# Kernel tuning notes

Hardware: AMD Instinct MI355X
Metric: run time of the kernel (lower is better)

The kernel has to match this reference:

```python
import jax, jax.numpy as jnp
from jax import lax
import numpy as np

NH, KA = 8, 3            # num_heads, local kernel size
C_HID = 64               # adapter hidden dim (== SlideAttention dim)
C_RED = C_HID // 4       # dim_reduction=4 -> 16
C_H = C_RED // NH        # channels per head after reduction -> 2
SCALE = float((C_HID // NH) ** -0.5)  # head_dim=8 scaling


def _shift_kernel(dtype):
    # fixed 'shift' depthwise kernel: output tap i picks neighbor (i//3, i%3)
    base = np.zeros((KA * KA, 1, KA, KA), np.float32)
    for i in range(KA * KA):
        base[i, 0, i // KA, i % KA] = 1.0
    return jnp.asarray(np.tile(base, (C_H, 1, 1, 1)), dtype)


def _dwconv(x, w, b):
    # depthwise grouped conv: (G, C_H, H, W) -> (G, C_H*9, H, W)
    y = lax.conv_general_dilated(x, w, (1, 1), 'SAME',
                                 dimension_numbers=('NCHW', 'OIHW', 'NCHW'),
                                 feature_group_count=C_H)
    return y + b[None, :, None, None]


def _forward(x, fc1_w, fc1_b, conv_w, conv_b, qkv_w, qkv_b, dep1_w, dep_b,
             dep1_b, rpb, proj_w, proj_b, fc2_w, fc2_b):
    B, L, _ = x.shape
    pw = lambda h, w, b: jnp.einsum('blc,oc->blo', h, w) + b  # 1x1 conv1d == pointwise linear
    xs = pw(x, fc1_w, fc1_b)                                   # (B,L,64)
    h = pw(pw(xs, conv_w[0], conv_b[0]), conv_w[1], conv_b[1])  # A,B (dropout=eval identity)
    h = pw(pw(h, conv_w[2], conv_b[2]), conv_w[3], conv_b[3])   # C,D
    h = pw(pw(h, conv_w[4], conv_b[4]), conv_w[5], conv_b[5])   # E,F
    h = pw(pw(h, conv_w[6], conv_b[6]), conv_w[7], conv_b[7]) + h  # G,H + residual (scale=1)
    xs = jax.nn.gelu(h, approximate=False)                     # nn.GELU default (erf)
    Hh, Ww, C = B, L, C_HID
    x4 = xs.reshape(1, C, Hh, Ww)                              # raw torch.reshape semantics
    # ---- SlideAttention (dim=64, heads=8, ka=3, dim_reduction=4, rpb) ----
    xp = jnp.transpose(x4, (0, 2, 3, 1))                       # (1,H,W,C)
    qkv = xp @ qkv_w.T + qkv_b                                 # (1,H,W,3*C_RED)
    f = jnp.transpose(qkv, (0, 3, 1, 2)).reshape(NH, 3 * C_H, Hh, Ww)
    q, k, v = f[:, :C_H], f[:, C_H:2 * C_H], f[:, 2 * C_H:]
    sw = _shift_kernel(x.dtype)
    k = _dwconv(k, sw, dep_b) + _dwconv(k, dep1_w, dep1_b)     # shared dwc kernels
    v = _dwconv(v, sw, dep_b) + _dwconv(v, dep1_w, dep1_b)
    q6 = q.reshape(1, NH, C_H, 1, Hh, Ww)
    k6 = k.reshape(1, NH, C_H, KA * KA, Hh, Ww) + rpb          # relative position bias
    v6 = v.reshape(1, NH, C_H, KA * KA, Hh, Ww)
    attn = jax.nn.softmax(jnp.sum(q6 * SCALE * k6, axis=2, keepdims=True), axis=3)
    o = jnp.sum(attn * v6, axis=3).reshape(1, C_RED, Hh, Ww)   # (1,16,H,W)
    o = jnp.transpose(o, (0, 2, 3, 1)) @ proj_w.T + proj_b     # (1,H,W,64)
    o = jnp.transpose(o, (0, 3, 1, 2))                         # (1,C,H,W)
    xs = o.reshape(Hh, Ww, C)                                  # raw reshape back
    out = xs @ fc2_w.T + fc2_b                                 # D_fc2: 64 -> 768
    return x + out                                             # skip connection


def setup_inputs() -> dict:
    ks = jax.random.split(jax.random.key(0), 16)
    f32 = jnp.float32
    n = lambda k, s, sc: jax.random.normal(k, s, f32) * sc
    return {
        'x': jax.random.normal(ks[0], (32, 2048, 768), f32),
        'fc1_w': n(ks[1], (64, 768), 0.05), 'fc1_b': n(ks[2], (64,), 0.02),
        'conv_w': n(ks[3], (8, 64, 64), 0.1), 'conv_b': n(ks[4], (8, 64), 0.02),
        'qkv_w': n(ks[5], (48, 64), 0.1), 'qkv_b': n(ks[6], (48,), 0.02),
        'dep1_w': n(ks[7], (18, 1, 3, 3), 0.1),
        'dep_b': n(ks[8], (18,), 0.02), 'dep1_b': n(ks[9], (18,), 0.02),
        'rpb': n(ks[10], (1, 8, 1, 9, 1, 1), 0.02),
        'proj_w': n(ks[11], (64, 16), 0.1), 'proj_b': n(ks[12], (64,), 0.02),
        'fc2_w': n(ks[13], (768, 64), 0.05), 'fc2_b': n(ks[14], (768,), 0.02),
    }


def reference(x, fc1_w, fc1_b, conv_w, conv_b, qkv_w, qkv_b, dep1_w, dep_b,
              dep1_b, rpb, proj_w, proj_b, fc2_w, fc2_b):
    return _forward(x, fc1_w, fc1_b, conv_w, conv_b, qkv_w, qkv_b, dep1_w,
                    dep_b, dep1_b, rpb, proj_w, proj_b, fc2_w, fc2_b)
```

## Files before the change

kernel.cpp:

```cpp
#include <hip/hip_runtime.h>
#include <math.h>

__device__ __forceinline__ int SW64(int ch, int t)  { return (ch << 6) + (t ^ (ch & 28)); }
__device__ __forceinline__ int SW128(int ch, int t) { return (ch << 7) + (t ^ (ch & 28)); }

__global__ __launch_bounds__(256, 4) void k_fc1_chain(
    const float* __restrict__ x, const float* __restrict__ fc1_w,
    const float* __restrict__ fc1_b, const float* __restrict__ conv_w,
    const float* __restrict__ conv_b, float* __restrict__ xs)
{
    __shared__ float lds[2 * 4096];
    float* bufA = lds;
    float* bufB = lds + 4096;

    const int tid = threadIdx.x;
    const int tx = tid & 15;
    const int ty = tid >> 4;
    const int t0 = blockIdx.x * 64;
    const int c0 = tx * 4;
    const int r0 = ty * 4;

    float acc[4][4];
#pragma unroll
    for (int i = 0; i < 4; ++i)
#pragma unroll
        for (int j = 0; j < 4; ++j) acc[i][j] = 0.f;

    float xr[4][4], wr1[4][4];
#pragma unroll
    for (int i = 0; i < 4; ++i) {
        const float4 v = *(const float4*)(x + (size_t)(t0 + r0 + i) * 768 + c0);
        xr[i][0] = v.x; xr[i][1] = v.y; xr[i][2] = v.z; xr[i][3] = v.w;
        const float4 u = *(const float4*)(fc1_w + (size_t)(r0 + i) * 768 + c0);
        wr1[i][0] = u.x; wr1[i][1] = u.y; wr1[i][2] = u.z; wr1[i][3] = u.w;
    }

    for (int k0 = 0; k0 < 768; k0 += 64) {
#pragma unroll
        for (int j = 0; j < 4; ++j) {
            float4 s; s.x = xr[0][j]; s.y = xr[1][j]; s.z = xr[2][j]; s.w = xr[3][j];
            *(float4*)(bufA + SW64(c0 + j, r0)) = s;
            float4 t; t.x = wr1[0][j]; t.y = wr1[1][j]; t.z = wr1[2][j]; t.w = wr1[3][j];
            *(float4*)(bufB + SW64(c0 + j, r0)) = t;
        }
        __syncthreads();

        if (k0 + 64 < 768) {
#pragma unroll
            for (int i = 0; i < 4; ++i) {
                const float4 v = *(const float4*)(x + (size_t)(t0 + r0 + i) * 768 + k0 + 64 + c0);
                xr[i][0] = v.x; xr[i][1] = v.y; xr[i][2] = v.z; xr[i][3] = v.w;
                const float4 u = *(const float4*)(fc1_w + (size_t)(r0 + i) * 768 + k0 + 64 + c0);
                wr1[i][0] = u.x; wr1[i][1] = u.y; wr1[i][2] = u.z; wr1[i][3] = u.w;
            }
        }

#pragma unroll 16
        for (int k = 0; k < 64; ++k) {
            const float4 a4 = *(const float4*)(bufA + SW64(k, r0));
            const float4 b4 = *(const float4*)(bufB + SW64(k, c0));
            const float a[4] = {a4.x, a4.y, a4.z, a4.w};
            const float b[4] = {b4.x, b4.y, b4.z, b4.w};
#pragma unroll
            for (int i = 0; i < 4; ++i)
#pragma unroll
                for (int j = 0; j < 4; ++j) acc[i][j] = fmaf(a[i], b[j], acc[i][j]);
        }
        __syncthreads();
    }

#pragma unroll
    for (int j = 0; j < 4; ++j) {
        const float b = fc1_b[c0 + j];
        float4 s;
        s.x = acc[0][j] + b; s.y = acc[1][j] + b;
        s.z = acc[2][j] + b; s.w = acc[3][j] + b;
        *(float4*)(bufA + SW64(c0 + j, r0)) = s;
    }
    {
        float wr[4][4];
#pragma unroll
        for (int i = 0; i < 4; ++i) {
            const float4 v = *(const float4*)(conv_w + (r0 + i) * 64 + c0);
            wr[i][0] = v.x; wr[i][1] = v.y; wr[i][2] = v.z; wr[i][3] = v.w;
        }
#pragma unroll
        for (int j = 0; j < 4; ++j) {
            float4 s; s.x = wr[0][j]; s.y = wr[1][j]; s.z = wr[2][j]; s.w = wr[3][j];
            *(float4*)(bufB + SW64(c0 + j, r0)) = s;
        }
    }
    __syncthreads();

    float* cur = bufA;
    float* wb  = bufB;
    float res[4][4];

    for (int l = 0; l < 8; ++l) {
        float wr[4][4];
        if (l < 7) {
#pragma unroll
            for (int i = 0; i < 4; ++i) {
                const float4 v = *(const float4*)(conv_w + (l + 1) * 4096 + (r0 + i) * 64 + c0);
                wr[i][0] = v.x; wr[i][1] = v.y; wr[i][2] = v.z; wr[i][3] = v.w;
            }
        }
#pragma unroll
        for (int i = 0; i < 4; ++i)
#pragma unroll
            for (int j = 0; j < 4; ++j) acc[i][j] = 0.f;
#pragma unroll 16
        for (int k = 0; k < 64; ++k) {
            const float4 a4 = *(const float4*)(cur + SW64(k, r0));
            const float4 b4 = *(const float4*)(wb + SW64(k, c0));
            const float a[4] = {a4.x, a4.y, a4.z, a4.w};
            const float b[4] = {b4.x, b4.y, b4.z, b4.w};
#pragma unroll
            for (int i = 0; i < 4; ++i)
#pragma unroll
                for (int j = 0; j < 4; ++j) acc[i][j] = fmaf(a[i], b[j], acc[i][j]);
        }
#pragma unroll
        for (int i = 0; i < 4; ++i)
#pragma unroll
            for (int j = 0; j < 4; ++j) acc[i][j] += conv_b[l * 64 + c0 + j];

        if (l == 5) {
#pragma unroll
            for (int i = 0; i < 4; ++i)
#pragma unroll
                for (int j = 0; j < 4; ++j) res[i][j] = acc[i][j];
        }
        if (l < 7) {
            __syncthreads();
#pragma unroll
            for (int j = 0; j < 4; ++j) {
                float4 s; s.x = acc[0][j]; s.y = acc[1][j]; s.z = acc[2][j]; s.w = acc[3][j];
                *(float4*)(wb + SW64(c0 + j, r0)) = s;
                float4 t; t.x = wr[0][j]; t.y = wr[1][j]; t.z = wr[2][j]; t.w = wr[3][j];
                *(float4*)(cur + SW64(c0 + j, r0)) = t;
            }
            float* tmp = cur; cur = wb; wb = tmp;
            __syncthreads();
        }
    }

#pragma unroll
    for (int i = 0; i < 4; ++i) {
        float4 g4;
        float v;
        v = acc[i][0] + res[i][0]; g4.x = 0.5f * v * (1.f + erff(v * 0.70710678118654752f));
        v = acc[i][1] + res[i][1]; g4.y = 0.5f * v * (1.f + erff(v * 0.70710678118654752f));
        v = acc[i][2] + res[i][2]; g4.z = 0.5f * v * (1.f + erff(v * 0.70710678118654752f));
        v = acc[i][3] + res[i][3]; g4.w = 0.5f * v * (1.f + erff(v * 0.70710678118654752f));
        *(float4*)(xs + (size_t)(t0 + r0 + i) * 64 + c0) = g4;
    }
}

__global__ __launch_bounds__(256) void k_qkv(
    const float* __restrict__ xs, const float* __restrict__ qkv_w,
    const float* __restrict__ qkv_b, float* __restrict__ qkv)
{
    __shared__ float wq[12 * 64];
    __shared__ float qb[12];
    const int tid = threadIdx.x;
    const int g = blockIdx.y;
    for (int i = tid; i < 768; i += 256) wq[i] = qkv_w[g * 768 + i];
    if (tid < 12) qb[tid] = qkv_b[g * 12 + tid];
    __syncthreads();

    const int p = blockIdx.x * 256 + tid;
    float acc[12];
#pragma unroll
    for (int n = 0; n < 12; ++n) acc[n] = qb[n];

    for (int c = 0; c < 64; c += 4) {
        const float xv0 = xs[(c + 0) * 65536 + p];
        const float xv1 = xs[(c + 1) * 65536 + p];
        const float xv2 = xs[(c + 2) * 65536 + p];
        const float xv3 = xs[(c + 3) * 65536 + p];
#pragma unroll
        for (int n = 0; n < 12; ++n) {
            const float4 w4 = *(const float4*)(wq + n * 64 + c);
            acc[n] += xv0 * w4.x + xv1 * w4.y + xv2 * w4.z + xv3 * w4.w;
        }
    }
#pragma unroll
    for (int n = 0; n < 12; ++n) qkv[(size_t)(g * 12 + n) * 65536 + p] = acc[n];
}

__global__ __launch_bounds__(256) void k_attn(
    const float* __restrict__ qkv, const float* __restrict__ dep1_w,
    const float* __restrict__ dep_b, const float* __restrict__ dep1_b,
    const float* __restrict__ rpb, const float* __restrict__ proj_w,
    const float* __restrict__ proj_b, float* __restrict__ obuf)
{
    __shared__ float s_d1w[162];
    __shared__ float s_db[18];
    __shared__ float s_d1b[18];
    __shared__ float s_rpb[72];
    __shared__ float s_pw[1024];
    __shared__ float s_pb[64];
    __shared__ float s_o[32 * 17];

    const int tid = threadIdx.x;
    if (tid < 162) s_d1w[tid] = dep1_w[tid];
    if (tid < 18) { s_db[tid] = dep_b[tid]; s_d1b[tid] = dep1_b[tid]; }
    if (tid < 72) s_rpb[tid] = rpb[tid];
    for (int i = tid; i < 1024; i += 256) s_pw[i] = proj_w[i];
    if (tid < 64) s_pb[tid] = proj_b[tid];
    __syncthreads();

    const int px = tid & 31;
    const int nh = tid >> 5;
    const int p = blockIdx.x * 32 + px;
    const int h = p >> 11;
    const int w = p & 2047;

    int np[9];
    float vmask[9];
#pragma unroll
    for (int t = 0; t < 9; ++t) {
        const int dh = t / 3 - 1, dw = t % 3 - 1;
        const int hh = h + dh, ww = w + dw;
        const bool ok = ((unsigned)hh < 32u) && ((unsigned)ww < 2048u);
        np[t] = ok ? (hh * 2048 + ww) : p;
        vmask[t] = ok ? 1.f : 0.f;
    }

    const float* base = qkv + nh * 6 * 65536;
    const float q0 = base[p];
    const float q1 = base[65536 + p];

    float kn[2][9];
#pragma unroll
    for (int c = 0; c < 2; ++c)
#pragma unroll
        for (int t = 0; t < 9; ++t)
            kn[c][t] = base[(2 + c) * 65536 + np[t]] * vmask[t];

    float lg[9];
#pragma unroll
    for (int i = 0; i < 9; ++i) {
        float s = 0.f;
#pragma unroll
        for (int c = 0; c < 2; ++c) {
            const int o = c * 9 + i;
            float conv = 0.f;
#pragma unroll
            for (int t = 0; t < 9; ++t) conv = fmaf(kn[c][t], s_d1w[o * 9 + t], conv);
            const float k6 = kn[c][i] + conv + s_db[o] + s_d1b[o] + s_rpb[nh * 9 + i];
            s = fmaf((c == 0 ? q0 : q1), k6, s);
        }
        lg[i] = s * 0.35355339059327373f;
    }
    float m = lg[0];
#pragma unroll
    for (int i = 1; i < 9; ++i) m = fmaxf(m, lg[i]);
    float sum = 0.f;
#pragma unroll
    for (int i = 0; i < 9; ++i) { lg[i] = expf(lg[i] - m); sum += lg[i]; }
    const float inv = 1.f / sum;

    float vn[2][9];
#pragma unroll
    for (int c = 0; c < 2; ++c)
#pragma unroll
        for (int t = 0; t < 9; ++t)
            vn[c][t] = base[(4 + c) * 65536 + np[t]] * vmask[t];

#pragma unroll
    for (int c = 0; c < 2; ++c) {
        float ov = 0.f;
#pragma unroll
        for (int i = 0; i < 9; ++i) {
            const int o = c * 9 + i;
            float conv = 0.f;
#pragma unroll
            for (int t = 0; t < 9; ++t) conv = fmaf(vn[c][t], s_d1w[o * 9 + t], conv);
            const float v6 = vn[c][i] + conv + s_db[o] + s_d1b[o];
            ov = fmaf(lg[i], v6, ov);
        }
        s_o[px * 17 + nh * 2 + c] = ov * inv;
    }
    __syncthreads();

    const int dg = tid >> 5;
    float my[16];
#pragma unroll
    for (int j = 0; j < 16; ++j) my[j] = s_o[px * 17 + j];
#pragma unroll
    for (int k = 0; k < 8; ++k) {
        const int d = dg * 8 + k;
        float s = s_pb[d];
#pragma unroll
        for (int j = 0; j < 16; ++j) s = fmaf(my[j], s_pw[d * 16 + j], s);
        obuf[(size_t)d * 65536 + p] = s;
    }
}

__global__ __launch_bounds__(256) void k_fc2(
    const float* __restrict__ ot, const float* __restrict__ fc2_w,
    const float* __restrict__ fc2_b, const float* __restrict__ x,
    float* __restrict__ out)
{
    __shared__ float As[64 * 64];
    __shared__ float Bs[64 * 128];

    const int tid = threadIdx.x;
    const int tx = tid & 15;
    const int ty = tid >> 4;
    const int t0 = blockIdx.x * 64;
    const int n0 = blockIdx.y * 128;
    const int c0 = tx * 4;
    const int r0 = ty * 4;

    {
        float ar[4][4];
#pragma unroll
        for (int i = 0; i < 4; ++i) {
            const float4 v = *(const float4*)(ot + (size_t)(t0 + r0 + i) * 64 + c0);
            ar[i][0] = v.x; ar[i][1] = v.y; ar[i][2] = v.z; ar[i][3] = v.w;
        }
#pragma unroll
        for (int j = 0; j < 4; ++j) {
            float4 s; s.x = ar[0][j]; s.y = ar[1][j]; s.z = ar[2][j]; s.w = ar[3][j];
            *(float4*)(As + SW64(c0 + j, r0)) = s;
        }
    }
#pragma unroll
    for (int half = 0; half < 2; ++half) {
        float br[4][4];
#pragma unroll
        for (int i = 0; i < 4; ++i) {
            const float4 v = *(const float4*)(fc2_w + (size_t)(n0 + half * 64 + r0 + i) * 64 + c0);
            br[i][0] = v.x; br[i][1] = v.y; br[i][2] = v.z; br[i][3] = v.w;
        }
#pragma unroll
        for (int j = 0; j < 4; ++j) {
            float4 s; s.x = br[0][j]; s.y = br[1][j]; s.z = br[2][j]; s.w = br[3][j];
            *(float4*)(Bs + SW128(c0 + j, half * 64 + r0)) = s;
        }
    }
    __syncthreads();

    float acc[4][8];
#pragma unroll
    for (int i = 0; i < 4; ++i)
#pragma unroll
        for (int j = 0; j < 8; ++j) acc[i][j] = 0.f;

#pragma unroll 8
    for (int k = 0; k < 64; ++k) {
        const float4 a4 = *(const float4*)(As + SW64(k, r0));
        const float4 b40 = *(const float4*)(Bs + SW128(k, c0));
        const float4 b41 = *(const float4*)(Bs + SW128(k, 64 + c0));
        const float a[4] = {a4.x, a4.y, a4.z, a4.w};
        const float b[8] = {b40.x, b40.y, b40.z, b40.w, b41.x, b41.y, b41.z, b41.w};
#pragma unroll
        for (int i = 0; i < 4; ++i)
#pragma unroll
            for (int j = 0; j < 8; ++j) acc[i][j] = fmaf(a[i], b[j], acc[i][j]);
    }

    float bb[8];
#pragma unroll
    for (int j = 0; j < 4; ++j) { bb[j] = fc2_b[n0 + c0 + j]; bb[4 + j] = fc2_b[n0 + 64 + c0 + j]; }

#pragma unroll
    for (int i = 0; i < 4; ++i) {
        const size_t off = (size_t)(t0 + r0 + i) * 768 + n0;
        const float4 x0 = *(const float4*)(x + off + c0);
        const float4 x1 = *(const float4*)(x + off + 64 + c0);
        float4 o0, o1;
        o0.x = acc[i][0] + bb[0] + x0.x;
        o0.y = acc[i][1] + bb[1] + x0.y;
        o0.z = acc[i][2] + bb[2] + x0.z;
        o0.w = acc[i][3] + bb[3] + x0.w;
        o1.x = acc[i][4] + bb[4] + x1.x;
        o1.y = acc[i][5] + bb[5] + x1.y;
        o1.z = acc[i][6] + bb[6] + x1.z;
        o1.w = acc[i][7] + bb[7] + x1.w;
        *(float4*)(out + off + c0) = o0;
        *(float4*)(out + off + 64 + c0) = o1;
    }
}

extern "C" void kernel_launch(void* const* d_in, const int* in_sizes, int n_in,
                              void* d_out, int out_size, void* d_ws, size_t ws_size,
                              hipStream_t stream) {
    const float* x      = (const float*)d_in[0];
    const float* fc1_w  = (const float*)d_in[1];
    const float* fc1_b  = (const float*)d_in[2];
    const float* conv_w = (const float*)d_in[3];
    const float* conv_b = (const float*)d_in[4];
    const float* qkv_w  = (const float*)d_in[5];
    const float* qkv_b  = (const float*)d_in[6];
    const float* dep1_w = (const float*)d_in[7];
    const float* dep_b  = (const float*)d_in[8];
    const float* dep1_b = (const float*)d_in[9];
    const float* rpb    = (const float*)d_in[10];
    const float* proj_w = (const float*)d_in[11];
    const float* proj_b = (const float*)d_in[12];
    const float* fc2_w  = (const float*)d_in[13];
    const float* fc2_b  = (const float*)d_in[14];

    float* ws   = (float*)d_ws;
    float* xs   = ws;
    float* qkv  = ws + 4194304;
    float* obuf = ws + 7340032;
    float* out  = (float*)d_out;

    k_fc1_chain<<<dim3(1024), dim3(256), 0, stream>>>(x, fc1_w, fc1_b, conv_w, conv_b, xs);
    k_qkv<<<dim3(256, 4), dim3(256), 0, stream>>>(xs, qkv_w, qkv_b, qkv);
    k_attn<<<dim3(2048), dim3(256), 0, stream>>>(qkv, dep1_w, dep_b, dep1_b, rpb,
                                                 proj_w, proj_b, obuf);
    k_fc2<<<dim3(1024, 6), dim3(256), 0, stream>>>(obuf, fc2_w, fc2_b, x, out);
}
```

Measured before the change: 588.4 us.

## Enlarge fc1-chain register tile to 8x8 and loop fc2 over all output columns per block

The fc1+conv chain kernel now handles 128 tokens per 128-thread block, with each thread computing an 8x8 output tile and a new XOR swizzle. This raises FMA work per LDS load and halves the per-token weight staging. The fc2 kernel now loops over all six 128-column chunks inside one block, so the A tile is staged once and the next weight chunk is prefetched into registers. The trade-off is lower occupancy: launch bounds of (128,1), heavy register use in the chain kernel, and only 512 and 1024 blocks launched.

```diff
diff --git a/kernel.cpp b/kernel.cpp
--- a/kernel.cpp
+++ b/kernel.cpp
@@ -1,159 +1,197 @@
 #include <hip/hip_runtime.h>
 #include <math.h>
 
+__device__ __forceinline__ int AIDX(int row, int t) {
+    return (row << 7) + (t ^ (((row >> 3) & 7) << 3));
+}
+__device__ __forceinline__ int WIDX(int k, int o) {
+    return (k << 6) + (o ^ (((k >> 3) & 7) << 3));
+}
 __device__ __forceinline__ int SW64(int ch, int t)  { return (ch << 6) + (t ^ (ch & 28)); }
 __device__ __forceinline__ int SW128(int ch, int t) { return (ch << 7) + (t ^ (ch & 28)); }
 
-__global__ __launch_bounds__(256, 4) void k_fc1_chain(
+__global__ __launch_bounds__(128, 1) void k_fc1_chain(
     const float* __restrict__ x, const float* __restrict__ fc1_w,
     const float* __restrict__ fc1_b, const float* __restrict__ conv_w,
     const float* __restrict__ conv_b, float* __restrict__ xs)
 {
-    __shared__ float lds[2 * 4096];
-    float* bufA = lds;
-    float* bufB = lds + 4096;
+    __shared__ float sA[64 * 128];
+    __shared__ float sW[64 * 64];
 
     const int tid = threadIdx.x;
-    const int tx = tid & 15;
-    const int ty = tid >> 4;
-    const int t0 = blockIdx.x * 64;
-    const int c0 = tx * 4;
-    const int r0 = ty * 4;
-
-    float acc[4][4];
-#pragma unroll
-    for (int i = 0; i < 4; ++i)
-#pragma unroll
-        for (int j = 0; j < 4; ++j) acc[i][j] = 0.f;
-
-    float xr[4][4], wr1[4][4];
-#pragma unroll
-    for (int i = 0; i < 4; ++i) {
-        const float4 v = *(const float4*)(x + (size_t)(t0 + r0 + i) * 768 + c0);
+    const int tx = tid & 7;
+    const int ty = tid >> 3;
+    const int c0 = tx * 8;
+    const int r0 = ty * 8;
+    const int t0 = blockIdx.x * 128;
+
+    const int k4 = (tid & 15) * 4;
+    const int tg = (tid >> 4) * 16;
+    const int og = tid >> 4;
+
+    float acc[8][8];
+    float xr[16][4];
+    float wr[8][4];
+
+#pragma unroll
+    for (int i = 0; i < 16; ++i) {
+        const float4 v = *(const float4*)(x + (size_t)(t0 + tg + i) * 768 + k4);
         xr[i][0] = v.x; xr[i][1] = v.y; xr[i][2] = v.z; xr[i][3] = v.w;
-        const float4 u = *(const float4*)(fc1_w + (size_t)(r0 + i) * 768 + c0);
-        wr1[i][0] = u.x; wr1[i][1] = u.y; wr1[i][2] = u.z; wr1[i][3] = u.w;
-    }
-
-    for (int k0 = 0; k0 < 768; k0 += 64) {
+    }
+#pragma unroll
+    for (int i = 0; i < 8; ++i) {
+        const float4 v = *(const float4*)(fc1_w + (size_t)(og * 8 + i) * 768 + k4);
+        wr[i][0] = v.x; wr[i][1] = v.y; wr[i][2] = v.z; wr[i][3] = v.w;
+    }
+#pragma unroll
+    for (int i = 0; i < 8; ++i)
+#pragma unroll
+        for (int j = 0; j < 8; ++j) acc[i][j] = 0.f;
+
+    for (int t = 0; t < 12; ++t) {
 #pragma unroll
         for (int j = 0; j < 4; ++j) {
-            float4 s; s.x = xr[0][j]; s.y = xr[1][j]; s.z = xr[2][j]; s.w = xr[3][j];
-            *(float4*)(bufA + SW64(c0 + j, r0)) = s;
-            float4 t; t.x = wr1[0][j]; t.y = wr1[1][j]; t.z = wr1[2][j]; t.w = wr1[3][j];
-            *(float4*)(bufB + SW64(c0 + j, r0)) = t;
+#pragma unroll
+            for (int q = 0; q < 4; ++q) {
+                float4 s = make_float4(xr[q*4+0][j], xr[q*4+1][j], xr[q*4+2][j], xr[q*4+3][j]);
+                *(float4*)(sA + AIDX(k4 + j, tg + q * 4)) = s;
+            }
+            float4 w0 = make_float4(wr[0][j], wr[1][j], wr[2][j], wr[3][j]);
+            float4 w1 = make_float4(wr[4][j], wr[5][j], wr[6][j], wr[7][j]);
+            *(float4*)(sW + WIDX(k4 + j, og * 8)) = w0;
+            *(float4*)(sW + WIDX(k4 + j, og * 8 + 4)) = w1;
         }
         __syncthreads();
 
-        if (k0 + 64 < 768) {
-#pragma unroll
-            for (int i = 0; i < 4; ++i) {
-                const float4 v = *(const float4*)(x + (size_t)(t0 + r0 + i) * 768 + k0 + 64 + c0);
+        const int kn = (t + 1) * 64;
+        if (t < 11) {
+#pragma unroll
+            for (int i = 0; i < 16; ++i) {
+                const float4 v = *(const float4*)(x + (size_t)(t0 + tg + i) * 768 + kn + k4);
                 xr[i][0] = v.x; xr[i][1] = v.y; xr[i][2] = v.z; xr[i][3] = v.w;
-                const float4 u = *(const float4*)(fc1_w + (size_t)(r0 + i) * 768 + k0 + 64 + c0);
-                wr1[i][0] = u.x; wr1[i][1] = u.y; wr1[i][2] = u.z; wr1[i][3] = u.w;
-            }
-        }
-
-#pragma unroll 16
+            }
+#pragma unroll
+            for (int i = 0; i < 8; ++i) {
+                const float4 v = *(const float4*)(fc1_w + (size_t)(og * 8 + i) * 768 + kn + k4);
+                wr[i][0] = v.x; wr[i][1] = v.y; wr[i][2] = v.z; wr[i][3] = v.w;
+            }
+        } else {
+#pragma unroll
+            for (int i = 0; i < 8; ++i) {
+                const float4 v = *(const float4*)(conv_w + (og * 8 + i) * 64 + k4);
+                wr[i][0] = v.x; wr[i][1] = v.y; wr[i][2] = v.z; wr[i][3] = v.w;
+            }
+        }
+
+#pragma unroll 4
         for (int k = 0; k < 64; ++k) {
-            const float4 a4 = *(const float4*)(bufA + SW64(k, r0));
-            const float4 b4 = *(const float4*)(bufB + SW64(k, c0));
-            const float a[4] = {a4.x, a4.y, a4.z, a4.w};
-            const float b[4] = {b4.x, b4.y, b4.z, b4.w};
-#pragma unroll
-            for (int i = 0; i < 4; ++i)
-#pragma unroll
-                for (int j = 0; j < 4; ++j) acc[i][j] = fmaf(a[i], b[j], acc[i][j]);
+            const int sw = ((k >> 3) & 7) << 3;
+            const float4 a0 = *(const float4*)(sA + (k << 7) + (r0 ^ sw));
+            const float4 a1 = *(const float4*)(sA + (k << 7) + ((r0 + 4) ^ sw));
+            const float4 b0 = *(const float4*)(sW + (k << 6) + (c0 ^ sw));
+            const float4 b1 = *(const float4*)(sW + (k << 6) + ((c0 + 4) ^ sw));
+            const float a[8] = {a0.x, a0.y, a0.z, a0.w, a1.x, a1.y, a1.z, a1.w};
+            const float b[8] = {b0.x, b0.y, b0.z, b0.w, b1.x, b1.y, b1.z, b1.w};
+#pragma unroll
+            for (int i = 0; i < 8; ++i)
+#pragma unroll
+                for (int j = 0; j < 8; ++j) acc[i][j] = fmaf(a[i], b[j], acc[i][j]);
         }
         __syncthreads();
     }
 
 #pragma unroll
+    for (int j = 0; j < 8; ++j) {
+        const float b = fc1_b[c0 + j];
+        float4 s0 = make_float4(acc[0][j] + b, acc[1][j] + b, acc[2][j] + b, acc[3][j] + b);
+        float4 s1 = make_float4(acc[4][j] + b, acc[5][j] + b, acc[6][j] + b, acc[7][j] + b);
+        *(float4*)(sA + AIDX(c0 + j, r0)) = s0;
+        *(float4*)(sA + AIDX(c0 + j, r0 + 4)) = s1;
+    }
+#pragma unroll
     for (int j = 0; j < 4; ++j) {
-        const float b = fc1_b[c0 + j];
-        float4 s;
-        s.x = acc[0][j] + b; s.y = acc[1][j] + b;
-        s.z = acc[2][j] + b; s.w = acc[3][j] + b;
-        *(float4*)(bufA + SW64(c0 + j, r0)) = s;
-    }
-    {
-        float wr[4][4];
-#pragma unroll
-        for (int i = 0; i < 4; ++i) {
-            const float4 v = *(const float4*)(conv_w + (r0 + i) * 64 + c0);
-            wr[i][0] = v.x; wr[i][1] = v.y; wr[i][2] = v.z; wr[i][3] = v.w;
-        }
-#pragma unroll
-        for (int j = 0; j < 4; ++j) {
-            float4 s; s.x = wr[0][j]; s.y = wr[1][j]; s.z = wr[2][j]; s.w = wr[3][j];
-            *(float4*)(bufB + SW64(c0 + j, r0)) = s;
-        }
+        float4 w0 = make_float4(wr[0][j], wr[1][j], wr[2][j], wr[3][j]);
+        float4 w1 = make_float4(wr[4][j], wr[5][j], wr[6][j], wr[7][j]);
+        *(float4*)(sW + WIDX(k4 + j, og * 8)) = w0;
+        *(float4*)(sW + WIDX(k4 + j, og * 8 + 4)) = w1;
     }
     __syncthreads();
 
-    float* cur = bufA;
-    float* wb  = bufB;
-    float res[4][4];
-
+    float res[8][8];
     for (int l = 0; l < 8; ++l) {
-        float wr[4][4];
         if (l < 7) {
 #pragma unroll
-            for (int i = 0; i < 4; ++i) {
-                const float4 v = *(const float4*)(conv_w + (l + 1) * 4096 + (r0 + i) * 64 + c0);
+            for (int i = 0; i < 8; ++i) {
+                const float4 v = *(const float4*)(conv_w + (l + 1) * 4096 + (og * 8 + i) * 64 + k4);
                 wr[i][0] = v.x; wr[i][1] = v.y; wr[i][2] = v.z; wr[i][3] = v.w;
             }
         }
 #pragma unroll
-        for (int i = 0; i < 4; ++i)
-#pragma unroll
-            for (int j = 0; j < 4; ++j) acc[i][j] = 0.f;
-#pragma unroll 16
+        for (int i = 0; i < 8; ++i)
+#pragma unroll
+            for (int j = 0; j < 8; ++j) acc[i][j] = 0.f;
+
+#pragma unroll 4
         for (int k = 0; k < 64; ++k) {
-            const float4 a4 = *(const float4*)(cur + SW64(k, r0));
-            const float4 b4 = *(const float4*)(wb + SW64(k, c0));
-            const float a[4] = {a4.x, a4.y, a4.z, a4.w};
-            const float b[4] = {b4.x, b4.y, b4.z, b4.w};
-#pragma unroll
-            for (int i = 0; i < 4; ++i)
-#pragma unroll
-                for (int j = 0; j < 4; ++j) acc[i][j] = fmaf(a[i], b[j], acc[i][j]);
-        }
-#pragma unroll
-        for (int i = 0; i < 4; ++i)
-#pragma unroll
-            for (int j = 0; j < 4; ++j) acc[i][j] += conv_b[l * 64 + c0 + j];
+            const int sw = ((k >> 3) & 7) << 3;
+            const float4 a0 = *(const float4*)(sA + (k << 7) + (r0 ^ sw));
+            const float4 a1 = *(const float4*)(sA + (k << 7) + ((r0 + 4) ^ sw));
+            const float4 b0 = *(const float4*)(sW + (k << 6) + (c0 ^ sw));
+            const float4 b1 = *(const float4*)(sW + (k << 6) + ((c0 + 4) ^ sw));
+            const float a[8] = {a0.x, a0.y, a0.z, a0.w, a1.x, a1.y, a1.z, a1.w};
+            const float b[8] = {b0.x, b0.y, b0.z, b0.w, b1.x, b1.y, b1.z, b1.w};
+#pragma unroll
+            for (int i = 0; i < 8; ++i)
+#pragma unroll
+                for (int j = 0; j < 8; ++j) acc[i][j] = fmaf(a[i], b[j], acc[i][j]);
+        }
+#pragma unroll
+        for (int j = 0; j < 8; ++j) {
+            const float b = conv_b[l * 64 + c0 + j];
+#pragma unroll
+            for (int i = 0; i < 8; ++i) acc[i][j] += b;
+        }
 
         if (l == 5) {
 #pragma unroll
-            for (int i = 0; i < 4; ++i)
-#pragma unroll
-                for (int j = 0; j < 4; ++j) res[i][j] = acc[i][j];
+            for (int i = 0; i < 8; ++i)
+#pragma unroll
+                for (int j = 0; j < 8; ++j) res[i][j] = acc[i][j];
         }
         if (l < 7) {
             __syncthreads();
 #pragma unroll
+            for (int j = 0; j < 8; ++j) {
+                float4 s0 = make_float4(acc[0][j], acc[1][j], acc[2][j], acc[3][j]);
+                float4 s1 = make_float4(acc[4][j], acc[5][j], acc[6][j], acc[7][j]);
+                *(float4*)(sA + AIDX(c0 + j, r0)) = s0;
+                *(float4*)(sA + AIDX(c0 + j, r0 + 4)) = s1;
+            }
+#pragma unroll
             for (int j = 0; j < 4; ++j) {
-                float4 s; s.x = acc[0][j]; s.y = acc[1][j]; s.z = acc[2][j]; s.w = acc[3][j];
-                *(float4*)(wb + SW64(c0 + j, r0)) = s;
-                float4 t; t.x = wr[0][j]; t.y = wr[1][j]; t.z = wr[2][j]; t.w = wr[3][j];
-                *(float4*)(cur + SW64(c0 + j, r0)) = t;
-            }
-            float* tmp = cur; cur = wb; wb = tmp;
+                float4 w0 = make_float4(wr[0][j], wr[1][j], wr[2][j], wr[3][j]);
+                float4 w1 = make_float4(wr[4][j], wr[5][j], wr[6][j], wr[7][j]);
+                *(float4*)(sW + WIDX(k4 + j, og * 8)) = w0;
+                *(float4*)(sW + WIDX(k4 + j, og * 8 + 4)) = w1;
+            }
             __syncthreads();
         }
     }
 
 #pragma unroll
-    for (int i = 0; i < 4; ++i) {
-        float4 g4;
+    for (int i = 0; i < 8; ++i) {
+        float4 g0, g1;
         float v;
-        v = acc[i][0] + res[i][0]; g4.x = 0.5f * v * (1.f + erff(v * 0.70710678118654752f));
-        v = acc[i][1] + res[i][1]; g4.y = 0.5f * v * (1.f + erff(v * 0.70710678118654752f));
-        v = acc[i][2] + res[i][2]; g4.z = 0.5f * v * (1.f + erff(v * 0.70710678118654752f));
-        v = acc[i][3] + res[i][3]; g4.w = 0.5f * v * (1.f + erff(v * 0.70710678118654752f));
-        *(float4*)(xs + (size_t)(t0 + r0 + i) * 64 + c0) = g4;
+        v = acc[i][0] + res[i][0]; g0.x = 0.5f * v * (1.f + erff(v * 0.70710678118654752f));
+        v = acc[i][1] + res[i][1]; g0.y = 0.5f * v * (1.f + erff(v * 0.70710678118654752f));
+        v = acc[i][2] + res[i][2]; g0.z = 0.5f * v * (1.f + erff(v * 0.70710678118654752f));
+        v = acc[i][3] + res[i][3]; g0.w = 0.5f * v * (1.f + erff(v * 0.70710678118654752f));
+        v = acc[i][4] + res[i][4]; g1.x = 0.5f * v * (1.f + erff(v * 0.70710678118654752f));
+        v = acc[i][5] + res[i][5]; g1.y = 0.5f * v * (1.f + erff(v * 0.70710678118654752f));
+        v = acc[i][6] + res[i][6]; g1.z = 0.5f * v * (1.f + erff(v * 0.70710678118654752f));
+        v = acc[i][7] + res[i][7]; g1.w = 0.5f * v * (1.f + erff(v * 0.70710678118654752f));
+        *(float4*)(xs + (size_t)(t0 + r0 + i) * 64 + c0) = g0;
+        *(float4*)(xs + (size_t)(t0 + r0 + i) * 64 + c0 + 4) = g1;
     }
 }
 
@@ -311,7 +349,6 @@
     const int tx = tid & 15;
     const int ty = tid >> 4;
     const int t0 = blockIdx.x * 64;
-    const int n0 = blockIdx.y * 128;
     const int c0 = tx * 4;
     const int r0 = ty * 4;
 
@@ -324,65 +361,82 @@
         }
 #pragma unroll
         for (int j = 0; j < 4; ++j) {
-            float4 s; s.x = ar[0][j]; s.y = ar[1][j]; s.z = ar[2][j]; s.w = ar[3][j];
+            float4 s = make_float4(ar[0][j], ar[1][j], ar[2][j], ar[3][j]);
             *(float4*)(As + SW64(c0 + j, r0)) = s;
         }
     }
-#pragma unroll
-    for (int half = 0; half < 2; ++half) {
-        float br[4][4];
+
+    float br[2][4][4];
+#pragma unroll
+    for (int half = 0; half < 2; ++half)
 #pragma unroll
         for (int i = 0; i < 4; ++i) {
-            const float4 v = *(const float4*)(fc2_w + (size_t)(n0 + half * 64 + r0 + i) * 64 + c0);
-            br[i][0] = v.x; br[i][1] = v.y; br[i][2] = v.z; br[i][3] = v.w;
-        }
-#pragma unroll
-        for (int j = 0; j < 4; ++j) {
-            float4 s; s.x = br[0][j]; s.y = br[1][j]; s.z = br[2][j]; s.w = br[3][j];
-            *(float4*)(Bs + SW128(c0 + j, half * 64 + r0)) = s;
-        }
-    }
-    __syncthreads();
-
-    float acc[4][8];
-#pragma unroll
-    for (int i = 0; i < 4; ++i)
-#pragma unroll
-        for (int j = 0; j < 8; ++j) acc[i][j] = 0.f;
+            const float4 v = *(const float4*)(fc2_w + (size_t)(half * 64 + r0 + i) * 64 + c0);
+            br[half][i][0] = v.x; br[half][i][1] = v.y; br[half][i][2] = v.z; br[half][i][3] = v.w;
+        }
+
+    for (int nc = 0; nc < 6; ++nc) {
+        const int n0 = nc * 128;
+#pragma unroll
+        for (int half = 0; half < 2; ++half)
+#pragma unroll
+            for (int j = 0; j < 4; ++j) {
+                float4 s = make_float4(br[half][0][j], br[half][1][j], br[half][2][j], br[half][3][j]);
+                *(float4*)(Bs + SW128(c0 + j, half * 64 + r0)) = s;
+            }
+        __syncthreads();
+
+        if (nc < 5) {
+#pragma unroll
+            for (int half = 0; half < 2; ++half)
+#pragma unroll
+                for (int i = 0; i < 4; ++i) {
+                    const float4 v = *(const float4*)(fc2_w + (size_t)(n0 + 128 + half * 64 + r0 + i) * 64 + c0);
+                    br[half][i][0] = v.x; br[half][i][1] = v.y; br[half][i][2] = v.z; br[half][i][3] = v.w;
+                }
+        }
+
+        float acc[4][8];
+#pragma unroll
+        for (int i = 0; i < 4; ++i)
+#pragma unroll
+            for (int j = 0; j < 8; ++j) acc[i][j] = 0.f;
 
 #pragma unroll 8
-    for (int k = 0; k < 64; ++k) {
-        const float4 a4 = *(const float4*)(As + SW64(k, r0));
-        const float4 b40 = *(const float4*)(Bs + SW128(k, c0));
-        const float4 b41 = *(const float4*)(Bs + SW128(k, 64 + c0));
-        const float a[4] = {a4.x, a4.y, a4.z, a4.w};
-        const float b[8] = {b40.x, b40.y, b40.z, b40.w, b41.x, b41.y, b41.z, b41.w};
-#pragma unroll
-        for (int i = 0; i < 4; ++i)
-#pragma unroll
-            for (int j = 0; j < 8; ++j) acc[i][j] = fmaf(a[i], b[j], acc[i][j]);
-    }
-
-    float bb[8];
-#pragma unroll
-    for (int j = 0; j < 4; ++j) { bb[j] = fc2_b[n0 + c0 + j]; bb[4 + j] = fc2_b[n0 + 64 + c0 + j]; }
-
-#pragma unroll
-    for (int i = 0; i < 4; ++i) {
-        const size_t off = (size_t)(t0 + r0 + i) * 768 + n0;
-        const float4 x0 = *(const float4*)(x + off + c0);
-        const float4 x1 = *(const float4*)(x + off + 64 + c0);
-        float4 o0, o1;
-        o0.x = acc[i][0] + bb[0] + x0.x;
-        o0.y = acc[i][1] + bb[1] + x0.y;
-        o0.z = acc[i][2] + bb[2] + x0.z;
-        o0.w = acc[i][3] + bb[3] + x0.w;
-        o1.x = acc[i][4] + bb[4] + x1.x;
-        o1.y = acc[i][5] + bb[5] + x1.y;
-        o1.z = acc[i][6] + bb[6] + x1.z;
-        o1.w = acc[i][7] + bb[7] + x1.w;
-        *(float4*)(out + off + c0) = o0;
-        *(float4*)(out + off + 64 + c0) = o1;
+        for (int k = 0; k < 64; ++k) {
+            const float4 a4  = *(const float4*)(As + SW64(k, r0));
+            const float4 b40 = *(const float4*)(Bs + SW128(k, c0));
+            const float4 b41 = *(const float4*)(Bs + SW128(k, 64 + c0));
+            const float a[4] = {a4.x, a4.y, a4.z, a4.w};
+            const float b[8] = {b40.x, b40.y, b40.z, b40.w, b41.x, b41.y, b41.z, b41.w};
+#pragma unroll
+            for (int i = 0; i < 4; ++i)
+#pragma unroll
+                for (int j = 0; j < 8; ++j) acc[i][j] = fmaf(a[i], b[j], acc[i][j]);
+        }
+
+        float bb[8];
+#pragma unroll
+        for (int j = 0; j < 4; ++j) { bb[j] = fc2_b[n0 + c0 + j]; bb[4 + j] = fc2_b[n0 + 64 + c0 + j]; }
+
+#pragma unroll
+        for (int i = 0; i < 4; ++i) {
+            const size_t off = (size_t)(t0 + r0 + i) * 768 + n0;
+            const float4 x0 = *(const float4*)(x + off + c0);
+            const float4 x1 = *(const float4*)(x + off + 64 + c0);
+            float4 o0, o1;
+            o0.x = acc[i][0] + bb[0] + x0.x;
+            o0.y = acc[i][1] + bb[1] + x0.y;
+            o0.z = acc[i][2] + bb[2] + x0.z;
+            o0.w = acc[i][3] + bb[3] + x0.w;
+            o1.x = acc[i][4] + bb[4] + x1.x;
+            o1.y = acc[i][5] + bb[5] + x1.y;
+            o1.z = acc[i][6] + bb[6] + x1.z;
+            o1.w = acc[i][7] + bb[7] + x1.w;
+            *(float4*)(out + off + c0) = o0;
+            *(float4*)(out + off + 64 + c0) = o1;
+        }
+        __syncthreads();
     }
 }
 
@@ -411,9 +465,9 @@
     float* obuf = ws + 7340032;
     float* out  = (float*)d_out;
 
-    k_fc1_chain<<<dim3(1024), dim3(256), 0, stream>>>(x, fc1_w, fc1_b, conv_w, conv_b, xs);
+    k_fc1_chain<<<dim3(512), dim3(128), 0, stream>>>(x, fc1_w, fc1_b, conv_w, conv_b, xs);
     k_qkv<<<dim3(256, 4), dim3(256), 0, stream>>>(xs, qkv_w, qkv_b, qkv);
     k_attn<<<dim3(2048), dim3(256), 0, stream>>>(qkv, dep1_w, dep_b, dep1_b, rpb,
                                                  proj_w, proj_b, obuf);
-    k_fc2<<<dim3(1024, 6), dim3(256), 0, stream>>>(obuf, fc2_w, fc2_b, x, out);
-}
+    k_fc2<<<dim3(1024), dim3(256), 0, stream>>>(obuf, fc2_w, fc2_b, x, out);
+}
```

Result: slower. 642.7 us (+9.2%).

## Replace XOR-swizzled LDS layouts with padded row-major tiles in fc1 chain and fc2

Applied to the files above, without the earlier changes.

The transposed, XOR-swizzled shared-memory layout for activations and weights becomes padded row-major tiles (pitch 68/132). A shared mm64 helper reads A rows as float4 over k and B rows per k, with coalesced row-wise loads of x for staging. The aim is fewer LDS bank conflicts and cheaper global loads and LDS stores, plus fewer LDS reads per FMA in the inner product. It uses more LDS and registers, which may lower occupancy for the 256-thread, 4-block-per-CU fc1 kernel. In fc2, the weights each thread stages are also reassigned.

```diff
diff --git a/kernel.cpp b/kernel.cpp
--- a/kernel.cpp
+++ b/kernel.cpp
@@ -1,103 +1,117 @@
 #include <hip/hip_runtime.h>
 #include <math.h>
 
-__device__ __forceinline__ int SW64(int ch, int t)  { return (ch << 6) + (t ^ (ch & 28)); }
-__device__ __forceinline__ int SW128(int ch, int t) { return (ch << 7) + (t ^ (ch & 28)); }
+#define P1 68
+#define PA 68
+#define PB 132
+
+__device__ __forceinline__ void mm64(const float* __restrict__ sA,
+                                     const float* __restrict__ sB,
+                                     int r0, int c0, float acc[4][4]) {
+#pragma unroll
+    for (int kq = 0; kq < 16; ++kq) {
+        float a[4][4];
+#pragma unroll
+        for (int i = 0; i < 4; ++i) {
+            const float4 v = *(const float4*)(sA + (r0 + i) * P1 + kq * 4);
+            a[i][0] = v.x; a[i][1] = v.y; a[i][2] = v.z; a[i][3] = v.w;
+        }
+#pragma unroll
+        for (int kk = 0; kk < 4; ++kk) {
+            const float4 b = *(const float4*)(sB + (kq * 4 + kk) * P1 + c0);
+            const float bb[4] = {b.x, b.y, b.z, b.w};
+#pragma unroll
+            for (int i = 0; i < 4; ++i)
+#pragma unroll
+                for (int j = 0; j < 4; ++j)
+                    acc[i][j] = fmaf(a[i][kk], bb[j], acc[i][j]);
+        }
+    }
+}
 
 __global__ __launch_bounds__(256, 4) void k_fc1_chain(
     const float* __restrict__ x, const float* __restrict__ fc1_w,
     const float* __restrict__ fc1_b, const float* __restrict__ conv_w,
     const float* __restrict__ conv_b, float* __restrict__ xs)
 {
-    __shared__ float lds[2 * 4096];
-    float* bufA = lds;
-    float* bufB = lds + 4096;
+    __shared__ float sAct[64 * P1];
+    __shared__ float sW[64 * P1];
 
     const int tid = threadIdx.x;
     const int tx = tid & 15;
     const int ty = tid >> 4;
-    const int t0 = blockIdx.x * 64;
     const int c0 = tx * 4;
     const int r0 = ty * 4;
-
+    const int t0 = blockIdx.x * 64;
+
+    const int arow = tid >> 2;
+    const int aq   = tid & 3;
+
+    float4 ar[4];
+    float wr[4][4];
     float acc[4][4];
+
+#pragma unroll
+    for (int j = 0; j < 4; ++j)
+        ar[j] = *(const float4*)(x + (size_t)(t0 + arow) * 768 + (aq + 4 * j) * 4);
+#pragma unroll
+    for (int i = 0; i < 4; ++i) {
+        const float4 v = *(const float4*)(fc1_w + (size_t)(r0 + i) * 768 + c0);
+        wr[i][0] = v.x; wr[i][1] = v.y; wr[i][2] = v.z; wr[i][3] = v.w;
+    }
 #pragma unroll
     for (int i = 0; i < 4; ++i)
 #pragma unroll
         for (int j = 0; j < 4; ++j) acc[i][j] = 0.f;
 
-    float xr[4][4], wr1[4][4];
-#pragma unroll
-    for (int i = 0; i < 4; ++i) {
-        const float4 v = *(const float4*)(x + (size_t)(t0 + r0 + i) * 768 + c0);
-        xr[i][0] = v.x; xr[i][1] = v.y; xr[i][2] = v.z; xr[i][3] = v.w;
-        const float4 u = *(const float4*)(fc1_w + (size_t)(r0 + i) * 768 + c0);
-        wr1[i][0] = u.x; wr1[i][1] = u.y; wr1[i][2] = u.z; wr1[i][3] = u.w;
-    }
-
-    for (int k0 = 0; k0 < 768; k0 += 64) {
-#pragma unroll
-        for (int j = 0; j < 4; ++j) {
-            float4 s; s.x = xr[0][j]; s.y = xr[1][j]; s.z = xr[2][j]; s.w = xr[3][j];
-            *(float4*)(bufA + SW64(c0 + j, r0)) = s;
-            float4 t; t.x = wr1[0][j]; t.y = wr1[1][j]; t.z = wr1[2][j]; t.w = wr1[3][j];
-            *(float4*)(bufB + SW64(c0 + j, r0)) = t;
-        }
+    for (int t = 0; t < 12; ++t) {
+#pragma unroll
+        for (int j = 0; j < 4; ++j)
+            *(float4*)(sAct + arow * P1 + (aq + 4 * j) * 4) = ar[j];
+#pragma unroll
+        for (int j = 0; j < 4; ++j)
+            *(float4*)(sW + (c0 + j) * P1 + r0) =
+                make_float4(wr[0][j], wr[1][j], wr[2][j], wr[3][j]);
         __syncthreads();
 
-        if (k0 + 64 < 768) {
+        if (t < 11) {
+            const int k0 = (t + 1) * 64;
+#pragma unroll
+            for (int j = 0; j < 4; ++j)
+                ar[j] = *(const float4*)(x + (size_t)(t0 + arow) * 768 + k0 + (aq + 4 * j) * 4);
 #pragma unroll
             for (int i = 0; i < 4; ++i) {
-                const float4 v = *(const float4*)(x + (size_t)(t0 + r0 + i) * 768 + k0 + 64 + c0);
-                xr[i][0] = v.x; xr[i][1] = v.y; xr[i][2] = v.z; xr[i][3] = v.w;
-                const float4 u = *(const float4*)(fc1_w + (size_t)(r0 + i) * 768 + k0 + 64 + c0);
-                wr1[i][0] = u.x; wr1[i][1] = u.y; wr1[i][2] = u.z; wr1[i][3] = u.w;
+                const float4 v = *(const float4*)(fc1_w + (size_t)(r0 + i) * 768 + k0 + c0);
+                wr[i][0] = v.x; wr[i][1] = v.y; wr[i][2] = v.z; wr[i][3] = v.w;
             }
-        }
-
-#pragma unroll 16
-        for (int k = 0; k < 64; ++k) {
-            const float4 a4 = *(const float4*)(bufA + SW64(k, r0));
-            const float4 b4 = *(const float4*)(bufB + SW64(k, c0));
-            const float a[4] = {a4.x, a4.y, a4.z, a4.w};
-            const float b[4] = {b4.x, b4.y, b4.z, b4.w};
-#pragma unroll
-            for (int i = 0; i < 4; ++i)
-#pragma unroll
-                for (int j = 0; j < 4; ++j) acc[i][j] = fmaf(a[i], b[j], acc[i][j]);
-        }
+        } else {
+#pragma unroll
+            for (int i = 0; i < 4; ++i) {
+                const float4 v = *(const float4*)(conv_w + (r0 + i) * 64 + c0);
+                wr[i][0] = v.x; wr[i][1] = v.y; wr[i][2] = v.z; wr[i][3] = v.w;
+            }
+        }
+
+        mm64(sAct, sW, r0, c0, acc);
         __syncthreads();
     }
 
-#pragma unroll
-    for (int j = 0; j < 4; ++j) {
-        const float b = fc1_b[c0 + j];
-        float4 s;
-        s.x = acc[0][j] + b; s.y = acc[1][j] + b;
-        s.z = acc[2][j] + b; s.w = acc[3][j] + b;
-        *(float4*)(bufA + SW64(c0 + j, r0)) = s;
-    }
     {
-        float wr[4][4];
-#pragma unroll
-        for (int i = 0; i < 4; ++i) {
-            const float4 v = *(const float4*)(conv_w + (r0 + i) * 64 + c0);
-            wr[i][0] = v.x; wr[i][1] = v.y; wr[i][2] = v.z; wr[i][3] = v.w;
-        }
-#pragma unroll
-        for (int j = 0; j < 4; ++j) {
-            float4 s; s.x = wr[0][j]; s.y = wr[1][j]; s.z = wr[2][j]; s.w = wr[3][j];
-            *(float4*)(bufB + SW64(c0 + j, r0)) = s;
-        }
-    }
+        const float4 b4 = *(const float4*)(fc1_b + c0);
+#pragma unroll
+        for (int i = 0; i < 4; ++i)
+            *(float4*)(sAct + (r0 + i) * P1 + c0) =
+                make_float4(acc[i][0] + b4.x, acc[i][1] + b4.y,
+                            acc[i][2] + b4.z, acc[i][3] + b4.w);
+    }
+#pragma unroll
+    for (int j = 0; j < 4; ++j)
+        *(float4*)(sW + (c0 + j) * P1 + r0) =
+            make_float4(wr[0][j], wr[1][j], wr[2][j], wr[3][j]);
     __syncthreads();
 
-    float* cur = bufA;
-    float* wb  = bufB;
     float res[4][4];
-
     for (int l = 0; l < 8; ++l) {
-        float wr[4][4];
         if (l < 7) {
 #pragma unroll
             for (int i = 0; i < 4; ++i) {
@@ -109,22 +123,17 @@
         for (int i = 0; i < 4; ++i)
 #pragma unroll
             for (int j = 0; j < 4; ++j) acc[i][j] = 0.f;
-#pragma unroll 16
-        for (int k = 0; k < 64; ++k) {
-            const float4 a4 = *(const float4*)(cur + SW64(k, r0));
-            const float4 b4 = *(const float4*)(wb + SW64(k, c0));
-            const float a[4] = {a4.x, a4.y, a4.z, a4.w};
-            const float b[4] = {b4.x, b4.y, b4.z, b4.w};
-#pragma unroll
-            for (int i = 0; i < 4; ++i)
-#pragma unroll
-                for (int j = 0; j < 4; ++j) acc[i][j] = fmaf(a[i], b[j], acc[i][j]);
-        }
-#pragma unroll
-        for (int i = 0; i < 4; ++i)
-#pragma unroll
-            for (int j = 0; j < 4; ++j) acc[i][j] += conv_b[l * 64 + c0 + j];
-
+
+        mm64(sAct, sW, r0, c0, acc);
+
+        {
+            const float4 b4 = *(const float4*)(conv_b + l * 64 + c0);
+#pragma unroll
+            for (int i = 0; i < 4; ++i) {
+                acc[i][0] += b4.x; acc[i][1] += b4.y;
+                acc[i][2] += b4.z; acc[i][3] += b4.w;
+            }
+        }
         if (l == 5) {
 #pragma unroll
             for (int i = 0; i < 4; ++i)
@@ -134,13 +143,13 @@
         if (l < 7) {
             __syncthreads();
 #pragma unroll
-            for (int j = 0; j < 4; ++j) {
-                float4 s; s.x = acc[0][j]; s.y = acc[1][j]; s.z = acc[2][j]; s.w = acc[3][j];
-                *(float4*)(wb + SW64(c0 + j, r0)) = s;
-                float4 t; t.x = wr[0][j]; t.y = wr[1][j]; t.z = wr[2][j]; t.w = wr[3][j];
-                *(float4*)(cur + SW64(c0 + j, r0)) = t;
-            }
-            float* tmp = cur; cur = wb; wb = tmp;
+            for (int i = 0; i < 4; ++i)
+                *(float4*)(sAct + (r0 + i) * P1 + c0) =
+                    make_float4(acc[i][0], acc[i][1], acc[i][2], acc[i][3]);
+#pragma unroll
+            for (int j = 0; j < 4; ++j)
+                *(float4*)(sW + (c0 + j) * P1 + r0) =
+                    make_float4(wr[0][j], wr[1][j], wr[2][j], wr[3][j]);
             __syncthreads();
         }
     }
@@ -304,8 +313,8 @@
     const float* __restrict__ fc2_b, const float* __restrict__ x,
     float* __restrict__ out)
 {
-    __shared__ float As[64 * 64];
-    __shared__ float Bs[64 * 128];
+    __shared__ float sA[64 * PA];
+    __shared__ float sB[64 * PB];
 
     const int tid = threadIdx.x;
     const int tx = tid & 15;
@@ -314,53 +323,56 @@
     const int n0 = blockIdx.y * 128;
     const int c0 = tx * 4;
     const int r0 = ty * 4;
-
-    {
-        float ar[4][4];
+    const int arow = tid >> 2;
+    const int aq   = tid & 3;
+
+    float4 av[4];
+#pragma unroll
+    for (int j = 0; j < 4; ++j)
+        av[j] = *(const float4*)(ot + (size_t)(t0 + arow) * 64 + (aq + 4 * j) * 4);
+    float bw[8][4];
+#pragma unroll
+    for (int i = 0; i < 8; ++i) {
+        const float4 v = *(const float4*)(fc2_w + (size_t)(n0 + ty * 8 + i) * 64 + c0);
+        bw[i][0] = v.x; bw[i][1] = v.y; bw[i][2] = v.z; bw[i][3] = v.w;
+    }
+#pragma unroll
+    for (int j = 0; j < 4; ++j)
+        *(float4*)(sA + arow * PA + (aq + 4 * j) * 4) = av[j];
+#pragma unroll
+    for (int j = 0; j < 4; ++j) {
+        *(float4*)(sB + (c0 + j) * PB + ty * 8) =
+            make_float4(bw[0][j], bw[1][j], bw[2][j], bw[3][j]);
+        *(float4*)(sB + (c0 + j) * PB + ty * 8 + 4) =
+            make_float4(bw[4][j], bw[5][j], bw[6][j], bw[7][j]);
+    }
+    __syncthreads();
+
+    float acc[4][8];
+#pragma unroll
+    for (int i = 0; i < 4; ++i)
+#pragma unroll
+        for (int j = 0; j < 8; ++j) acc[i][j] = 0.f;
+
+#pragma unroll
+    for (int kq = 0; kq < 16; ++kq) {
+        float a[4][4];
 #pragma unroll
         for (int i = 0; i < 4; ++i) {
-            const float4 v = *(const float4*)(ot + (size_t)(t0 + r0 + i) * 64 + c0);
-            ar[i][0] = v.x; ar[i][1] = v.y; ar[i][2] = v.z; ar[i][3] = v.w;
-        }
-#pragma unroll
-        for (int j = 0; j < 4; ++j) {
-            float4 s; s.x = ar[0][j]; s.y = ar[1][j]; s.z = ar[2][j]; s.w = ar[3][j];
-            *(float4*)(As + SW64(c0 + j, r0)) = s;
-        }
-    }
-#pragma unroll
-    for (int half = 0; half < 2; ++half) {
-        float br[4][4];
-#pragma unroll
-        for (int i = 0; i < 4; ++i) {
-            const float4 v = *(const float4*)(fc2_w + (size_t)(n0 + half * 64 + r0 + i) * 64 + c0);
-            br[i][0] = v.x; br[i][1] = v.y; br[i][2] = v.z; br[i][3] = v.w;
-        }
-#pragma unroll
-        for (int j = 0; j < 4; ++j) {
-            float4 s; s.x = br[0][j]; s.y = br[1][j]; s.z = br[2][j]; s.w = br[3][j];
-            *(float4*)(Bs + SW128(c0 + j, half * 64 + r0)) = s;
-        }
-    }
-    __syncthreads();
-
-    float acc[4][8];
-#pragma unroll
-    for (int i = 0; i < 4; ++i)
-#pragma unroll
-        for (int j = 0; j < 8; ++j) acc[i][j] = 0.f;
-
-#pragma unroll 8
-    for (int k = 0; k < 64; ++k) {
-        const float4 a4 = *(const float4*)(As + SW64(k, r0));
-        const float4 b40 = *(const float4*)(Bs + SW128(k, c0));
-        const float4 b41 = *(const float4*)(Bs + SW128(k, 64 + c0));
-        const float a[4] = {a4.x, a4.y, a4.z, a4.w};
-        const float b[8] = {b40.x, b40.y, b40.z, b40.w, b41.x, b41.y, b41.z, b41.w};
-#pragma unroll
-        for (int i = 0; i < 4; ++i)
-#pragma unroll
-            for (int j = 0; j < 8; ++j) acc[i][j] = fmaf(a[i], b[j], acc[i][j]);
+            const float4 v = *(const float4*)(sA + (r0 + i) * PA + kq * 4);
+            a[i][0] = v.x; a[i][1] = v.y; a[i][2] = v.z; a[i][3] = v.w;
+        }
+#pragma unroll
+        for (int kk = 0; kk < 4; ++kk) {
+            const float4 b0 = *(const float4*)(sB + (kq * 4 + kk) * PB + c0);
+            const float4 b1 = *(const float4*)(sB + (kq * 4 + kk) * PB + 64 + c0);
+            const float b[8] = {b0.x, b0.y, b0.z, b0.w, b1.x, b1.y, b1.z, b1.w};
+#pragma unroll
+            for (int i = 0; i < 4; ++i)
+#pragma unroll
+                for (int j = 0; j < 8; ++j)
+                    acc[i][j] = fmaf(a[i][kk], b[j], acc[i][j]);
+        }
     }
 
     float bb[8];
```

Result: slower. 712.0 us (+21.0%).
